# Optimization experiments

Measured on AMD Instinct MI355X. Metric: run time of the kernel, lower is better.

## Reference

```python
import jax, jax.numpy as jnp
import numpy as np
from jax import lax

B, S, D, H = 8, 1024, 512, 8
K = 25  # moving-average kernel
EPS = 1e-6


def setup_inputs() -> dict:
    key = jax.random.key(0)
    ks = jax.random.split(key, 8)

    def dense_w(k, din, dout):
        return (jax.random.normal(k, (din, dout), jnp.float32) / np.sqrt(din).astype(np.float32))

    return {
        "x": jax.random.normal(ks[0], (B, S, D), jnp.float32),
        "wq": dense_w(ks[1], D, D), "bq": jnp.zeros((D,), jnp.float32),
        "wk": dense_w(ks[2], D, D), "bk": jnp.zeros((D,), jnp.float32),
        "wv": dense_w(ks[3], D, D), "bv": jnp.zeros((D,), jnp.float32),
        "wo": dense_w(ks[4], D, D), "bo": jnp.zeros((D,), jnp.float32),
        "w1": dense_w(ks[5], D, 4 * D), "b1": jnp.zeros((4 * D,), jnp.float32),
        "w2": dense_w(ks[6], 4 * D, D), "b2": jnp.zeros((D,), jnp.float32),
        "g1": jnp.ones((D,), jnp.float32), "be1": jnp.zeros((D,), jnp.float32),
        "g2": jnp.ones((D,), jnp.float32), "be2": jnp.zeros((D,), jnp.float32),
        "g3": jnp.ones((D,), jnp.float32), "be3": jnp.zeros((D,), jnp.float32),
        "num_heads": H,
    }


def _moving_avg(x):
    # TF AveragePooling1D(pool=K, stride=1, padding='same'): divisor excludes padding.
    s = lax.reduce_window(x, 0.0, lax.add, (1, K, 1), (1, 1, 1), 'SAME')
    cnt = lax.reduce_window(jnp.ones((1, x.shape[1], 1), x.dtype), 0.0, lax.add,
                            (1, K, 1), (1, 1, 1), 'SAME')
    return s / cnt


def _layernorm(x, g, b):
    m = jnp.mean(x, -1, keepdims=True)
    v = jnp.var(x, -1, keepdims=True)
    return (x - m) * jax.lax.rsqrt(v + EPS) * g + b


def _auto_correlation(x, wq, bq, wk, bk, wv, bv, wo, bo, num_heads):
    b, s, d = x.shape
    dp = d // num_heads
    def split_heads(t):
        return t.reshape(b, s, num_heads, dp).transpose(0, 2, 1, 3)  # [B,H,S,dp]
    q = split_heads(x @ wq + bq)
    k = split_heads(x @ wk + bk)
    v = split_heads(x @ wv + bv)
    # Faithful to source: rfft over innermost (depth) axis, fft_length = 2*S.
    qf = jnp.fft.rfft(q, n=2 * s, axis=-1)
    kf = jnp.fft.rfft(k, n=2 * s, axis=-1)
    corr = jnp.fft.irfft(qf * jnp.conj(kf), n=2 * s, axis=-1)[..., :s]  # [B,H,S,S]
    scale = 1.0 / np.sqrt(dp).astype(np.float32)
    attn = jax.nn.softmax(scale * corr, axis=-1)
    out = jnp.einsum('bhst,bhtd->bhsd', attn, v)
    out = out.transpose(0, 2, 1, 3).reshape(b, s, d)
    return out @ wo + bo


def reference(x, wq, bq, wk, bk, wv, bv, wo, bo, w1, b1, w2, b2,
              g1, be1, g2, be2, g3, be3, num_heads):
    trend_init = _moving_avg(x)
    seasonal_init = x - trend_init
    attn_out = _auto_correlation(seasonal_init, wq, bq, wk, bk, wv, bv, wo, bo, num_heads)
    out1 = _layernorm(attn_out + seasonal_init, g1, be1)
    ffn = jax.nn.relu(out1 @ w1 + b1) @ w2 + b2
    seasonal_out = _layernorm(out1 + ffn, g2, be2) + seasonal_init
    trend2 = _moving_avg(seasonal_out)
    seasonal_final = seasonal_out - trend2
    x_out = seasonal_final + (trend2 + trend_init)
    return _layernorm(x_out, g3, be3)
```

## Files before the change

kernel.cpp:

```cpp
#include <hip/hip_runtime.h>
#include <cstdint>


typedef float f32x4 __attribute__((ext_vector_type(4)));
typedef __bf16 bf16x8 __attribute__((ext_vector_type(8)));
typedef _Float16 h2t __attribute__((ext_vector_type(2)));
typedef unsigned short u16;
typedef unsigned int u32;
typedef u32 u32x4 __attribute__((ext_vector_type(4)));

__device__ __forceinline__ u16 f2bf(float f) {
  unsigned int u = __float_as_uint(f);
  u = (u + 0x7FFFu + ((u >> 16) & 1u)) >> 16;
  return (u16)u;
}

__device__ __forceinline__ float bf2f(u16 b) { return __uint_as_float((u32)b << 16); }

__device__ __forceinline__ u16 f2h(float f) {
  _Float16 hv = (_Float16)f;
  u16 b;
  __builtin_memcpy(&b, &hv, 2);
  return b;
}

__device__ __forceinline__ float dot2h(u32 qp, u32 kp_, float c) {
#if __has_builtin(__builtin_amdgcn_fdot2)
  return __builtin_amdgcn_fdot2(__builtin_bit_cast(h2t, qp),
                                __builtin_bit_cast(h2t, kp_), c, false);
#else
  h2t q = __builtin_bit_cast(h2t, qp), k = __builtin_bit_cast(h2t, kp_);
  c = fmaf((float)q.x, (float)k.x, c);
  return fmaf((float)q.y, (float)k.y, c);
#endif
}

__device__ __forceinline__ void gload_lds16(const void* g, void* l) {
  __builtin_amdgcn_global_load_lds((__attribute__((address_space(1))) void*)g,
                                   (__attribute__((address_space(3))) void*)l,
                                   16, 0, 0);
}

__global__ __launch_bounds__(256) void prep_kernel(
    const float* __restrict__ wq, const float* __restrict__ wk,
    const float* __restrict__ wv, const float* __restrict__ wo,
    const float* __restrict__ w1, const float* __restrict__ w2,
    const float* __restrict__ bq, const float* __restrict__ bk,
    u16* __restrict__ wqkt, u16* __restrict__ wvt, u16* __restrict__ wot,
    u16* __restrict__ w1t, u16* __restrict__ w2t, float* __restrict__ qkbias,
    const float* __restrict__ x, u16* __restrict__ seas_bf,
    u16* __restrict__ a64, float* __restrict__ srow) {
  __shared__ float tile[32][33];
  int i = blockIdx.x;
  int tid = threadIdx.x;
  int tx = tid & 31, ty = tid >> 5;
  if (i >= 3076) {
    int blk = i - 3076;
    int sc = blk & 127, b = blk >> 7;
    int d = tid * 2;
    const float* xb = x + (size_t)b * 1024 * 512 + d;
    int s0 = sc * 8;
    int lo = max(s0 - 12, 0), hi = min(s0 + 12, 1023);
    float sx = 0.f, sy = 0.f;
    for (int j = lo; j <= hi; ++j) {
      float2 v = *(const float2*)&xb[(size_t)j * 512];
      sx += v.x;
      sy += v.y;
    }
    float ax = 0.f, ay = 0.f;
#pragma unroll
    for (int s = s0; s < s0 + 8; ++s) {
      int l2 = max(s - 12, 0), h2 = min(s + 12, 1023);
      float invc = 1.f / (float)(h2 - l2 + 1);
      float2 xv = *(const float2*)&xb[(size_t)s * 512];
      float sex = xv.x - sx * invc;
      float sey = xv.y - sy * invc;
      size_t idx = (size_t)(b * 1024 + s) * 512 + d;
      u32 pk = (u32)f2bf(sex) | ((u32)f2bf(sey) << 16);
      *(u32*)&seas_bf[idx] = pk;
      if (s < 64) *(u32*)&a64[(size_t)(b * 64 + s) * 512 + d] = pk;
      ax += sex;
      ay += sey;
      if (s - 12 >= 0) {
        float2 v = *(const float2*)&xb[(size_t)(s - 12) * 512];
        sx -= v.x;
        sy -= v.y;
      }
      if (s + 13 <= 1023) {
        float2 v = *(const float2*)&xb[(size_t)(s + 13) * 512];
        sx += v.x;
        sy += v.y;
      }
    }
    atomicAdd(&srow[b * 512 + d], ax);
    atomicAdd(&srow[b * 512 + d + 1], ay);
    return;
  }
  if (i >= 3072) {
    int idx = (i - 3072) * 256 + tid;
    qkbias[idx] = idx < 512 ? bq[idx] : bk[idx - 512];
    return;
  }
  const float* src;
  u16* dst;
  int R, C, bx, by;
  if (i < 1024) {
    int w = i >> 8, l = i & 255;
    src = (w == 0 ? wq : w == 1 ? wk : w == 2 ? wv : wo);
    dst = (w == 0 ? wqkt : w == 1 ? wqkt + 512 * 512 : w == 2 ? wvt : wot);
    R = 512; C = 512; bx = l & 15; by = l >> 4;
  } else if (i < 2048) {
    int l = i - 1024;
    src = w1; dst = w1t; R = 512; C = 2048; bx = l & 15; by = l >> 4;
  } else {
    int l = i - 2048;
    src = w2; dst = w2t; R = 2048; C = 512; bx = l & 63; by = l >> 6;
  }
  int r0 = bx * 32, c0 = by * 32;
#pragma unroll
  for (int k = 0; k < 4; ++k)
    tile[ty + 8 * k][tx] = src[(size_t)(r0 + ty + 8 * k) * C + c0 + tx];
  __syncthreads();
#pragma unroll
  for (int k = 0; k < 4; ++k)
    dst[(size_t)(c0 + ty + 8 * k) * R + r0 + tx] = f2bf(tile[tx][ty + 8 * k]);
}

__global__ __launch_bounds__(256) void vsum_kernel(
    const float* __restrict__ srow, const float* __restrict__ wv,
    const float* __restrict__ bv, float* __restrict__ vsum) {
  int blk = blockIdx.x;
  int b = blk >> 1;
  int n = (blk & 1) * 256 + threadIdx.x;
  float a0 = 0.f, a1 = 0.f, a2 = 0.f, a3 = 0.f;
  float a4 = 0.f, a5 = 0.f, a6 = 0.f, a7 = 0.f;
  const float* sr = srow + b * 512;
  for (int k = 0; k < 512; k += 8) {
    a0 = fmaf(sr[k + 0], wv[(size_t)(k + 0) * 512 + n], a0);
    a1 = fmaf(sr[k + 1], wv[(size_t)(k + 1) * 512 + n], a1);
    a2 = fmaf(sr[k + 2], wv[(size_t)(k + 2) * 512 + n], a2);
    a3 = fmaf(sr[k + 3], wv[(size_t)(k + 3) * 512 + n], a3);
    a4 = fmaf(sr[k + 4], wv[(size_t)(k + 4) * 512 + n], a4);
    a5 = fmaf(sr[k + 5], wv[(size_t)(k + 5) * 512 + n], a5);
    a6 = fmaf(sr[k + 6], wv[(size_t)(k + 6) * 512 + n], a6);
    a7 = fmaf(sr[k + 7], wv[(size_t)(k + 7) * 512 + n], a7);
  }
  vsum[b * 512 + n] = ((a0 + a1) + (a2 + a3)) + ((a4 + a5) + (a6 + a7)) + 1024.f * bv[n];
}

template <int RELU, int OMODE, int KSPLIT>
__global__ __launch_bounds__(512, 1) void gemm8p_kernel(
    const u16* __restrict__ A, const u16* __restrict__ Bt,
    const float* __restrict__ bias, void* __restrict__ Cv, void* __restrict__ Cv2,
    int M, int N, int K) {
  __shared__ u16 As[3][2][256 * 32];
  __shared__ u16 Bs[3][2][128 * 32];
  const int tid = threadIdx.x;
  const int wid = tid >> 6, lane = tid & 63;
  const int wm = wid >> 2, wn = wid & 3;
  const int la = lane & 15, lg = lane >> 4;
  int nwg = gridDim.x * gridDim.y;
  int lin = blockIdx.y * gridDim.x + blockIdx.x;
  int swz = (lin & 7) * (nwg >> 3) + (lin >> 3);
  int bx = swz / gridDim.y, by = swz % gridDim.y;
  const int row0 = bx * 256, col0 = by * 128;
  const int z = (KSPLIT > 1) ? (int)blockIdx.z : 0;
  const int kbeg = z * (K / KSPLIT);
  const int nt = (K / KSPLIT) / 64;
  f32x4 acc[8][2] = {};

  auto stageh = [&](int buf, int h, int k0) {
    int kh = k0 + h * 32;
    {
      int p = tid, r = p >> 2, cg = (p & 3) ^ ((r >> 1) & 3);
      gload_lds16(A + (size_t)(row0 + r) * K + kh + cg * 8,
                  ((char*)&As[buf][h][0]) + p * 16);
    }
    {
      int p = tid + 512, r = p >> 2, cg = (p & 3) ^ ((r >> 1) & 3);
      gload_lds16(A + (size_t)(row0 + r) * K + kh + cg * 8,
                  ((char*)&As[buf][h][0]) + p * 16);
    }
    {
      int p = tid, r = p >> 2, cg = (p & 3) ^ ((r >> 1) & 3);
      gload_lds16(Bt + (size_t)(col0 + r) * K + kh + cg * 8,
                  ((char*)&Bs[buf][h][0]) + p * 16);
    }
  };

  stageh(0, 0, kbeg);
  stageh(0, 1, kbeg);
  stageh(1, 0, kbeg + 64);
  stageh(1, 1, kbeg + 64);
  asm volatile("s_waitcnt vmcnt(6)" ::: "memory");
  __builtin_amdgcn_s_barrier();
  __builtin_amdgcn_sched_barrier(0);

  for (int t = 0; t < nt; ++t) {
    const int buf = t % 3;
    const int nbuf = (t + 2) % 3;
    const bool pre = (t + 2 < nt);
#pragma unroll
    for (int h = 0; h < 2; ++h) {
      bf16x8 af[8], bf[2];
#pragma unroll
      for (int mf = 0; mf < 8; ++mf) {
        int r = wm * 128 + mf * 16 + la;
        int cp = lg ^ ((r >> 1) & 3);
        af[mf] = *(const bf16x8*)&As[buf][h][r * 32 + cp * 8];
      }
#pragma unroll
      for (int nf = 0; nf < 2; ++nf) {
        int r = wn * 32 + nf * 16 + la;
        int cp = lg ^ ((r >> 1) & 3);
        bf[nf] = *(const bf16x8*)&Bs[buf][h][r * 32 + cp * 8];
      }
      if (pre) stageh(nbuf, h, kbeg + (t + 2) * 64);
      __builtin_amdgcn_sched_barrier(0);
      __builtin_amdgcn_s_barrier();
      __builtin_amdgcn_s_setprio(1);
#pragma unroll
      for (int mf = 0; mf < 8; ++mf)
#pragma unroll
        for (int nf = 0; nf < 2; ++nf)
          acc[mf][nf] = __builtin_amdgcn_mfma_f32_16x16x32_bf16(af[mf], bf[nf], acc[mf][nf], 0, 0, 0);
      __builtin_amdgcn_s_setprio(0);
      __builtin_amdgcn_sched_barrier(0);
      if (h == 0) __builtin_amdgcn_s_barrier();
    }
    if (pre)
      asm volatile("s_waitcnt vmcnt(6)" ::: "memory");
    else if (t + 1 < nt)
      asm volatile("s_waitcnt vmcnt(0)" ::: "memory");
    __builtin_amdgcn_s_barrier();
    __builtin_amdgcn_sched_barrier(0);
  }

  void* Cout = (z == 0) ? Cv : Cv2;
#pragma unroll
  for (int mf = 0; mf < 8; ++mf) {
    int r = row0 + wm * 128 + mf * 16 + lg * 4;
#pragma unroll
    for (int nf = 0; nf < 2; ++nf) {
      int cc = col0 + wn * 32 + nf * 16 + la;
      float bvv = (z == 0) ? bias[cc] : 0.f;
#pragma unroll
      for (int j = 0; j < 4; ++j) {
        float v = acc[mf][nf][j] + bvv;
        if (RELU) v = fmaxf(v, 0.f);
        if constexpr (OMODE == 1)
          ((u16*)Cout)[(size_t)(r + j) * N + cc] = f2bf(v);
        else
          ((u16*)Cout)[(size_t)(r + j) * N + cc] = f2h(v);
      }
    }
  }
}

template <int RELU>
__global__ __launch_bounds__(512, 1) void gemm256_kernel(
    const u16* __restrict__ A, const u16* __restrict__ Bt,
    const float* __restrict__ bias, u16* __restrict__ C, int M, int N, int K) {
  constexpr int BK = 32;
  __shared__ u16 As[3][256 * BK];
  __shared__ u16 Bs[3][256 * BK];
  const int tid = threadIdx.x;
  const int wid = tid >> 6, lane = tid & 63;
  const int wm = wid >> 2, wn = wid & 3;
  const int la = lane & 15, lg = lane >> 4;
  int nwg = gridDim.x * gridDim.y;
  int lin = blockIdx.y * gridDim.x + blockIdx.x;
  int swz = (lin & 7) * (nwg >> 3) + (lin >> 3);
  int bx = swz / gridDim.y, by = swz % gridDim.y;
  const int row0 = bx * 256, col0 = by * 256;
  const int nt = K / BK;
  f32x4 acc[8][4] = {};

  auto stage = [&](int buf, int k0) {
#pragma unroll
    for (int j = 0; j < 2; ++j) {
      int p = tid + j * 512;
      int r = p >> 2, cg = (p & 3) ^ ((r >> 1) & 3);
      gload_lds16(A + (size_t)(row0 + r) * K + k0 + cg * 8, ((char*)As[buf]) + p * 16);
      gload_lds16(Bt + (size_t)(col0 + r) * K + k0 + cg * 8, ((char*)Bs[buf]) + p * 16);
    }
  };

  stage(0, 0);
  stage(1, BK);
  asm volatile("s_waitcnt vmcnt(4)" ::: "memory");
  __builtin_amdgcn_s_barrier();
  __builtin_amdgcn_sched_barrier(0);

  for (int t = 0; t < nt; ++t) {
    const int cur = t % 3;
    if (t + 2 < nt) stage((t + 2) % 3, (t + 2) * BK);
    __builtin_amdgcn_sched_barrier(0);
    bf16x8 af[8], bfr[4];
#pragma unroll
    for (int mf = 0; mf < 8; ++mf) {
      int r = wm * 128 + mf * 16 + la;
      int cp = lg ^ ((r >> 1) & 3);
      af[mf] = *(const bf16x8*)(((const char*)As[cur]) + r * 64 + cp * 16);
    }
#pragma unroll
    for (int nf = 0; nf < 4; ++nf) {
      int r = wn * 64 + nf * 16 + la;
      int cp = lg ^ ((r >> 1) & 3);
      bfr[nf] = *(const bf16x8*)(((const char*)Bs[cur]) + r * 64 + cp * 16);
    }
    __builtin_amdgcn_s_setprio(1);
#pragma unroll
    for (int mf = 0; mf < 8; ++mf)
#pragma unroll
      for (int nf = 0; nf < 4; ++nf)
        acc[mf][nf] = __builtin_amdgcn_mfma_f32_16x16x32_bf16(af[mf], bfr[nf], acc[mf][nf], 0, 0, 0);
    __builtin_amdgcn_s_setprio(0);
    if (t + 2 < nt)
      asm volatile("s_waitcnt vmcnt(4)" ::: "memory");
    else
      asm volatile("s_waitcnt vmcnt(0)" ::: "memory");
    __builtin_amdgcn_s_barrier();
    __builtin_amdgcn_sched_barrier(0);
  }

#pragma unroll
  for (int mf = 0; mf < 8; ++mf) {
    int r = row0 + wm * 128 + mf * 16 + lg * 4;
#pragma unroll
    for (int nf = 0; nf < 4; ++nf) {
      int cc = col0 + wn * 64 + nf * 16 + la;
      float bvv = bias[cc];
#pragma unroll
      for (int j = 0; j < 4; ++j) {
        float v = acc[mf][nf][j] + bvv;
        if (RELU) v = fmaxf(v, 0.f);
        C[(size_t)(r + j) * N + cc] = f2bf(v);
      }
    }
  }
}

__global__ __launch_bounds__(256, 6) void gemm_v_kernel(
    const u16* __restrict__ A, const u16* __restrict__ Bt,
    const float* __restrict__ bias, u16* __restrict__ Cv, int M, int N, int K) {
  constexpr int BK = 32;
  __shared__ u16 As[2][128 * BK];
  __shared__ u16 Bs[2][64 * BK];
  const int tid = threadIdx.x;
  const int wid = tid >> 6, lane = tid & 63;
  const int wm = wid >> 1, wn = wid & 1;
  const int la = lane & 15, lg = lane >> 4;
  const int row0 = blockIdx.x * 128, col0 = blockIdx.y * 64;
  const int ksteps = K / BK;
  f32x4 acc[4][2] = {};

  auto stage = [&](int buf, int k0) {
    {
      int p = tid, r = p >> 2, cg = (p & 3) ^ ((r >> 1) & 3);
      gload_lds16(A + (size_t)(row0 + r) * K + k0 + cg * 8, ((char*)As[buf]) + p * 16);
    }
    {
      int p = tid + 256, r = p >> 2, cg = (p & 3) ^ ((r >> 1) & 3);
      gload_lds16(A + (size_t)(row0 + r) * K + k0 + cg * 8, ((char*)As[buf]) + p * 16);
    }
    {
      int p = tid, r = p >> 2, cg = (p & 3) ^ ((r >> 1) & 3);
      gload_lds16(Bt + (size_t)(col0 + r) * K + k0 + cg * 8, ((char*)Bs[buf]) + p * 16);
    }
  };

  stage(0, 0);
  __syncthreads();
  for (int t = 0; t < ksteps; ++t) {
    const int cur = t & 1;
    if (t + 1 < ksteps) stage(cur ^ 1, (t + 1) * BK);
    bf16x8 af[4], bfr[2];
#pragma unroll
    for (int m = 0; m < 4; ++m) {
      int r = wm * 64 + m * 16 + la;
      int cp = lg ^ ((r >> 1) & 3);
      af[m] = *(const bf16x8*)(((const char*)As[cur]) + r * 64 + cp * 16);
    }
#pragma unroll
    for (int n = 0; n < 2; ++n) {
      int r = wn * 32 + n * 16 + la;
      int cp = lg ^ ((r >> 1) & 3);
      bfr[n] = *(const bf16x8*)(((const char*)Bs[cur]) + r * 64 + cp * 16);
    }
#pragma unroll
    for (int m = 0; m < 4; ++m)
#pragma unroll
      for (int n = 0; n < 2; ++n)
        acc[m][n] = __builtin_amdgcn_mfma_f32_16x16x32_bf16(af[m], bfr[n], acc[m][n], 0, 0, 0);
    __syncthreads();
  }

#pragma unroll
  for (int m = 0; m < 4; ++m) {
    int r = row0 + wm * 64 + m * 16 + lg * 4;
#pragma unroll
    for (int n = 0; n < 2; ++n) {
      int cc = col0 + wn * 32 + n * 16 + la;
      float bvv = bias[cc];
#pragma unroll
      for (int j = 0; j < 4; ++j) {
        float v = acc[m][n][j] + bvv;
        int rr = r + j;
        int bb = rr >> 6, tt = rr & 63, hh = cc >> 6, dd = cc & 63;
        Cv[(((size_t)bb * 8 + hh) * 64 + dd) * 64 + tt] = f2bf(v);
      }
    }
  }
}

__global__ __launch_bounds__(256) void attn_mfma_kernel(
    const u16* __restrict__ qk, const u16* __restrict__ v64t,
    const float* __restrict__ vsum, u16* __restrict__ attn_bf) {
  __shared__ u32 qE[16][64];
  __shared__ u32 qO[16][64];
  __shared__ u32 kp[16][32];
  __shared__ u16 coef[16][64];
  __shared__ u16 vtt[64][64];
  __shared__ float zc[16];
  __shared__ float Vs[64];
  int bid = blockIdx.x;
  int scnk = bid & 63, h = (bid >> 6) & 7, b = bid >> 9;
  int tid = threadIdx.x, wid = tid >> 6, lane = tid & 63;
  int bh = b * 8 + h;
  int row0 = b * 1024 + scnk * 16;

  {
    int p = tid, r = p >> 3, cc = p & 7;
    gload_lds16(v64t + ((size_t)bh * 4096 + r * 64 + ((cc ^ (r & 7)) * 8)),
                ((char*)vtt) + p * 16);
    p = tid + 256; r = p >> 3; cc = p & 7;
    gload_lds16(v64t + ((size_t)bh * 4096 + r * 64 + ((cc ^ (r & 7)) * 8)),
                ((char*)vtt) + p * 16);
  }
  for (int idx = tid; idx < 512; idx += 256) {
    int s = idx >> 5, j = (idx & 31) + 32;
    qE[s][j] = 0;
  }
  {
    if (tid < 128) {
      int s = tid >> 3, c = tid & 7;
      size_t grow = ((size_t)(row0 + s)) * 1024 + h * 64;
      *(f32x4*)&qE[s][c * 4] = *(const f32x4*)&qk[grow + c * 8];
    } else {
      int t2 = tid - 128;
      int s = t2 >> 3, c = t2 & 7;
      size_t grow = ((size_t)(row0 + s)) * 1024 + 512 + h * 64;
      *(f32x4*)&kp[s][c * 4] = *(const f32x4*)&qk[grow + c * 8];
    }
  }
  if (tid < 64) Vs[tid] = vsum[b * 512 + h * 64 + tid];
  __syncthreads();
  for (int idx = tid; idx < 512; idx += 256) {
    int s = idx >> 5, j = idx & 31;
    u32 a = qE[s][j], b2 = qE[s][j + 1];
    qO[s][j] = (a >> 16) | (b2 << 16);
    qO[s][j + 32] = 0;
  }
  __syncthreads();
  for (int i = 0; i < 4; ++i) {
    int s = wid * 4 + i;
    u32x4 kk4[8];
#pragma unroll
    for (int u = 0; u < 8; ++u) kk4[u] = *(const u32x4*)&kp[s][u * 4];
    int t = lane, sel = t & 1;
    const u32* qptr = (sel ? qO[s] : qE[s]) + (t >> 1);
    float c = 0.f;
#pragma unroll
    for (int u = 0; u < 8; ++u) {
#pragma unroll
      for (int v = 0; v < 4; ++v) c = dot2h(qptr[u * 4 + v], kk4[u][v], c);
    }
    float sc = c * 0.125f;
    float mx = fmaxf(sc, 0.f);
#pragma unroll
    for (int off = 32; off >= 1; off >>= 1) mx = fmaxf(mx, __shfl_xor(mx, off));
    float w = __expf(sc - mx), wz = __expf(-mx);
    float sw = w;
#pragma unroll
    for (int off = 32; off >= 1; off >>= 1) sw += __shfl_xor(sw, off);
    float inv = 1.f / (sw + 960.f * wz);
    *(u16*)(((char*)&coef[s][0]) + ((2 * t) ^ ((s & 7) << 4))) = f2bf((w - wz) * inv);
    if (lane == 0) zc[s] = wz * inv;
  }
  __syncthreads();
  {
    int la = lane & 15, lg = lane >> 4;
    int r = la;
    int n0 = wid * 16 + la;
    f32x4 a0 = {};
#pragma unroll
    for (int ks = 0; ks < 2; ++ks) {
      int lr = ks * 4 + lg;
      bf16x8 af = *(const bf16x8*)(((const char*)coef) + r * 128 + ((lr ^ (r & 7)) << 4));
      bf16x8 b0 = *(const bf16x8*)(((const char*)vtt) + n0 * 128 + ((lr ^ (n0 & 7)) << 4));
      a0 = __builtin_amdgcn_mfma_f32_16x16x32_bf16(af, b0, a0, 0, 0, 0);
    }
    int srl0 = lg * 4;
    float vs0 = Vs[wid * 16 + la];
#pragma unroll
    for (int j = 0; j < 4; ++j) {
      size_t rb = (size_t)(row0 + srl0 + j) * 512 + h * 64;
      attn_bf[rb + wid * 16 + la] = f2bf(a0[j] + zc[srl0 + j] * vs0);
    }
  }
}

__device__ __forceinline__ void block_reduce_2(float& a, float& b, float* sbuf) {
  int tid = threadIdx.x, wid = tid >> 6, lane = tid & 63;
#pragma unroll
  for (int off = 32; off >= 1; off >>= 1) {
    a += __shfl_xor(a, off);
    b += __shfl_xor(b, off);
  }
  if (lane == 0) {
    sbuf[wid] = a;
    sbuf[4 + wid] = b;
  }
  __syncthreads();
  a = sbuf[0] + sbuf[1] + sbuf[2] + sbuf[3];
  b = sbuf[4] + sbuf[5] + sbuf[6] + sbuf[7];
  __syncthreads();
}

__global__ __launch_bounds__(256) void ln_res_kernel(
    const u16* __restrict__ xa, const u16* __restrict__ xb,
    u16* __restrict__ res_out,
    const float* __restrict__ g, const float* __restrict__ be) {
  __shared__ float sbuf[8];
  int row = blockIdx.x, tid = threadIdx.x;
  int d = tid * 2;
  size_t base = (size_t)row * 512 + d;
  u32 pa = *(const u32*)&xa[base];
  u32 pb = *(const u32*)&xb[base];
  u32 pr = *(const u32*)&res_out[base];
  float v0 = bf2f((u16)pa) + bf2f((u16)pb) + bf2f((u16)pr);
  float v1 = bf2f((u16)(pa >> 16)) + bf2f((u16)(pb >> 16)) + bf2f((u16)(pr >> 16));
  float s = v0 + v1, q = v0 * v0 + v1 * v1;
  block_reduce_2(s, q, sbuf);
  float mean = s * (1.f / 512.f);
  float var = q * (1.f / 512.f) - mean * mean;
  float rs = rsqrtf(var + 1e-6f);
  float2 gg = *(const float2*)&g[d];
  float2 bb = *(const float2*)&be[d];
  float o0 = (v0 - mean) * rs * gg.x + bb.x;
  float o1 = (v1 - mean) * rs * gg.y + bb.y;
  *(u32*)&res_out[base] = (u32)f2bf(o0) | ((u32)f2bf(o1) << 16);
}

__global__ __launch_bounds__(256) void final_kernel(
    const u16* __restrict__ out1, const u16* __restrict__ fa,
    const u16* __restrict__ fb, const float* __restrict__ x,
    const float* __restrict__ g2, const float* __restrict__ be2,
    const float* __restrict__ g3, const float* __restrict__ be3,
    float* __restrict__ out) {
  __shared__ float sbuf[8];
  int row = blockIdx.x, tid = threadIdx.x;
  int d = tid * 2;
  size_t base = (size_t)row * 512 + d;
  u32 po = *(const u32*)&out1[base];
  u32 pa = *(const u32*)&fa[base];
  u32 pb = *(const u32*)&fb[base];
  float t0 = bf2f((u16)po) + bf2f((u16)pa) + bf2f((u16)pb);
  float t1 = bf2f((u16)(po >> 16)) + bf2f((u16)(pa >> 16)) + bf2f((u16)(pb >> 16));
  float s = t0 + t1, q = t0 * t0 + t1 * t1;
  block_reduce_2(s, q, sbuf);
  float mean = s * (1.f / 512.f);
  float var = q * (1.f / 512.f) - mean * mean;
  float rs = rsqrtf(var + 1e-6f);
  float2 g2v = *(const float2*)&g2[d];
  float2 b2v = *(const float2*)&be2[d];
  float2 xv = *(const float2*)&x[base];
  float y0 = (t0 - mean) * rs * g2v.x + b2v.x + xv.x;
  float y1 = (t1 - mean) * rs * g2v.y + b2v.y + xv.y;
  s = y0 + y1;
  q = y0 * y0 + y1 * y1;
  block_reduce_2(s, q, sbuf);
  mean = s * (1.f / 512.f);
  var = q * (1.f / 512.f) - mean * mean;
  rs = rsqrtf(var + 1e-6f);
  float2 g3v = *(const float2*)&g3[d];
  float2 b3v = *(const float2*)&be3[d];
  float2 o = make_float2((y0 - mean) * rs * g3v.x + b3v.x,
                         (y1 - mean) * rs * g3v.y + b3v.y);
  *(float2*)&out[base] = o;
}

extern "C" void kernel_launch(void* const* d_in, const int* in_sizes, int n_in,
                              void* d_out, int out_size, void* d_ws, size_t ws_size,
                              hipStream_t stream) {
  const float* x = (const float*)d_in[0];
  const float* wq = (const float*)d_in[1];
  const float* bq = (const float*)d_in[2];
  const float* wk = (const float*)d_in[3];
  const float* bk = (const float*)d_in[4];
  const float* wv = (const float*)d_in[5];
  const float* bv = (const float*)d_in[6];
  const float* wo = (const float*)d_in[7];
  const float* bo = (const float*)d_in[8];
  const float* w1 = (const float*)d_in[9];
  const float* b1 = (const float*)d_in[10];
  const float* w2 = (const float*)d_in[11];
  const float* b2 = (const float*)d_in[12];
  const float* g1 = (const float*)d_in[13];
  const float* be1 = (const float*)d_in[14];
  const float* g2 = (const float*)d_in[15];
  const float* be2 = (const float*)d_in[16];
  const float* g3 = (const float*)d_in[17];
  const float* be3 = (const float*)d_in[18];
  float* out = (float*)d_out;

  const size_t MS = 8192ull * 512ull;
  float* srow = (float*)d_ws;
  float* vsumb = srow + 4096;
  float* qkbias = vsumb + 4096;
  u16* qk_f16 = (u16*)(qkbias + 1024);
  u16* hidden = qk_f16 + 8192ull * 1024;
  u16* seas_bf = hidden + 8192ull * 2048;
  u16* attn_bf = seas_bf + MS;
  u16* wo0 = attn_bf + MS;
  u16* wo1 = wo0 + MS;
  u16* v64t = wo1 + MS;
  u16* a64_bf = v64t + 512 * 512;
  u16* wqkt = a64_bf + 512 * 512;
  u16* wvt = wqkt + 1024 * 512;
  u16* wot = wvt + 512 * 512;
  u16* w1t = wot + 512 * 512;
  u16* w2t = w1t + 2048ull * 512;
  u16* ff0 = qk_f16;
  u16* ff1 = ff0 + MS;

  hipMemsetAsync(srow, 0, 4096 * sizeof(float), stream);
  prep_kernel<<<4100, 256, 0, stream>>>(
      wq, wk, wv, wo, w1, w2, bq, bk, wqkt, wvt, wot, w1t, w2t, qkbias,
      x, seas_bf, a64_bf, srow);
  vsum_kernel<<<16, 256, 0, stream>>>(srow, wv, bv, vsumb);

  gemm8p_kernel<0, 2, 1><<<dim3(32, 8), 512, 0, stream>>>(
      seas_bf, wqkt, qkbias, qk_f16, nullptr, 8192, 1024, 512);
  gemm_v_kernel<<<dim3(4, 8), 256, 0, stream>>>(a64_bf, wvt, bv, v64t, 512, 512, 512);

  attn_mfma_kernel<<<4096, 256, 0, stream>>>(qk_f16, v64t, vsumb, attn_bf);

  gemm8p_kernel<0, 1, 2><<<dim3(32, 4, 2), 512, 0, stream>>>(
      attn_bf, wot, bo, wo0, wo1, 8192, 512, 512);
  ln_res_kernel<<<8192, 256, 0, stream>>>(wo0, wo1, seas_bf, g1, be1);

  gemm256_kernel<1><<<dim3(32, 8), 512, 0, stream>>>(
      seas_bf, w1t, b1, hidden, 8192, 2048, 512);
  gemm8p_kernel<0, 1, 2><<<dim3(32, 4, 2), 512, 0, stream>>>(
      hidden, w2t, b2, ff0, ff1, 8192, 512, 2048);

  final_kernel<<<8192, 256, 0, stream>>>(seas_bf, ff0, ff1, x, g2, be2, g3, be3, out);
}
```

Baseline: 203.5 us.

## Rewrite FFN GEMMs with ping-pong 64-wide K pipeline and 4-way split-K for W2

Replaces the triple-buffered 256x256 GEMM with a double-buffered kernel that stages 64-wide K chunks as two 32-wide sub-slabs. Global loads for the next chunk are interleaved between half-tile MFMA phases, with barriers and priority hints around each phase, so that loads overlap compute. The same kernel now also runs the second FFN GEMM as a 4-way split-K over 256x256 tiles, replacing the 2-way gemm8p launch. The extra partial outputs reuse the wo0/wo1 buffers and are summed in final_kernel. The aim is better load/compute overlap and more workgroups for the K=2048 GEMM, at the cost of extra bf16 partial-sum traffic and barriers.

```diff
diff --git a/kernel.cpp b/kernel.cpp
--- a/kernel.cpp
+++ b/kernel.cpp
@@ -257,13 +257,13 @@
   }
 }
 
-template <int RELU>
-__global__ __launch_bounds__(512, 1) void gemm256_kernel(
+template <int RELU, int KSPLIT>
+__global__ __launch_bounds__(512, 1) void gemmfp_kernel(
     const u16* __restrict__ A, const u16* __restrict__ Bt,
-    const float* __restrict__ bias, u16* __restrict__ C, int M, int N, int K) {
-  constexpr int BK = 32;
-  __shared__ u16 As[3][256 * BK];
-  __shared__ u16 Bs[3][256 * BK];
+    const float* __restrict__ bias, u16* __restrict__ C0, u16* __restrict__ C1,
+    u16* __restrict__ C2, u16* __restrict__ C3, int M, int N, int K) {
+  __shared__ u16 As[2][2][256 * 32];
+  __shared__ u16 Bs[2][2][256 * 32];
   const int tid = threadIdx.x;
   const int wid = tid >> 6, lane = tid & 63;
   const int wm = wid >> 2, wn = wid & 3;
@@ -273,69 +273,111 @@
   int swz = (lin & 7) * (nwg >> 3) + (lin >> 3);
   int bx = swz / gridDim.y, by = swz % gridDim.y;
   const int row0 = bx * 256, col0 = by * 256;
-  const int nt = K / BK;
+  const int z = (KSPLIT > 1) ? (int)blockIdx.z : 0;
+  const int kbeg = z * (K / KSPLIT);
+  const int nt = (K / KSPLIT) / 64;
   f32x4 acc[8][4] = {};
 
-  auto stage = [&](int buf, int k0) {
+  auto stageA = [&](int d, int s, int k0) {
 #pragma unroll
     for (int j = 0; j < 2; ++j) {
       int p = tid + j * 512;
       int r = p >> 2, cg = (p & 3) ^ ((r >> 1) & 3);
-      gload_lds16(A + (size_t)(row0 + r) * K + k0 + cg * 8, ((char*)As[buf]) + p * 16);
-      gload_lds16(Bt + (size_t)(col0 + r) * K + k0 + cg * 8, ((char*)Bs[buf]) + p * 16);
+      gload_lds16(A + (size_t)(row0 + r) * K + k0 + s * 32 + cg * 8,
+                  ((char*)&As[d][s][0]) + p * 16);
     }
   };
-
-  stage(0, 0);
-  stage(1, BK);
-  asm volatile("s_waitcnt vmcnt(4)" ::: "memory");
+  auto stageB = [&](int d, int s, int k0) {
+#pragma unroll
+    for (int j = 0; j < 2; ++j) {
+      int p = tid + j * 512;
+      int r = p >> 2, cg = (p & 3) ^ ((r >> 1) & 3);
+      gload_lds16(Bt + (size_t)(col0 + r) * K + k0 + s * 32 + cg * 8,
+                  ((char*)&Bs[d][s][0]) + p * 16);
+    }
+  };
+
+  stageA(0, 0, kbeg);
+  stageB(0, 0, kbeg);
+  stageA(0, 1, kbeg);
+  stageB(0, 1, kbeg);
+  asm volatile("s_waitcnt vmcnt(0)" ::: "memory");
   __builtin_amdgcn_s_barrier();
   __builtin_amdgcn_sched_barrier(0);
 
   for (int t = 0; t < nt; ++t) {
-    const int cur = t % 3;
-    if (t + 2 < nt) stage((t + 2) % 3, (t + 2) * BK);
-    __builtin_amdgcn_sched_barrier(0);
-    bf16x8 af[8], bfr[4];
-#pragma unroll
-    for (int mf = 0; mf < 8; ++mf) {
-      int r = wm * 128 + mf * 16 + la;
-      int cp = lg ^ ((r >> 1) & 3);
-      af[mf] = *(const bf16x8*)(((const char*)As[cur]) + r * 64 + cp * 16);
-    }
-#pragma unroll
-    for (int nf = 0; nf < 4; ++nf) {
-      int r = wn * 64 + nf * 16 + la;
-      int cp = lg ^ ((r >> 1) & 3);
-      bfr[nf] = *(const bf16x8*)(((const char*)Bs[cur]) + r * 64 + cp * 16);
-    }
-    __builtin_amdgcn_s_setprio(1);
-#pragma unroll
-    for (int mf = 0; mf < 8; ++mf)
-#pragma unroll
-      for (int nf = 0; nf < 4; ++nf)
-        acc[mf][nf] = __builtin_amdgcn_mfma_f32_16x16x32_bf16(af[mf], bfr[nf], acc[mf][nf], 0, 0, 0);
-    __builtin_amdgcn_s_setprio(0);
-    if (t + 2 < nt)
-      asm volatile("s_waitcnt vmcnt(4)" ::: "memory");
-    else
-      asm volatile("s_waitcnt vmcnt(0)" ::: "memory");
-    __builtin_amdgcn_s_barrier();
-    __builtin_amdgcn_sched_barrier(0);
-  }
-
+    const int d = t & 1, nd = d ^ 1;
+    const int k1 = kbeg + (t + 1) * 64;
+    const bool pre = (t + 1 < nt);
+    bf16x8 af[8], bf[2];
+#pragma unroll
+    for (int s = 0; s < 2; ++s) {
+#pragma unroll
+      for (int mf = 0; mf < 8; ++mf) {
+        int r = wm * 128 + mf * 16 + la;
+        int cp = lg ^ ((r >> 1) & 3);
+        af[mf] = *(const bf16x8*)(((const char*)&As[d][s][0]) + r * 64 + cp * 16);
+      }
+#pragma unroll
+      for (int nf = 0; nf < 2; ++nf) {
+        int r = wn * 64 + nf * 16 + la;
+        int cp = lg ^ ((r >> 1) & 3);
+        bf[nf] = *(const bf16x8*)(((const char*)&Bs[d][s][0]) + r * 64 + cp * 16);
+      }
+      if (pre) stageA(nd, s, k1);
+      __builtin_amdgcn_sched_barrier(0);
+      __builtin_amdgcn_s_barrier();
+      asm volatile("s_waitcnt lgkmcnt(0)" ::: "memory");
+      __builtin_amdgcn_sched_barrier(0);
+      __builtin_amdgcn_s_setprio(1);
+#pragma unroll
+      for (int mf = 0; mf < 8; ++mf)
+#pragma unroll
+        for (int nf = 0; nf < 2; ++nf)
+          acc[mf][nf] = __builtin_amdgcn_mfma_f32_16x16x32_bf16(af[mf], bf[nf], acc[mf][nf], 0, 0, 0);
+      __builtin_amdgcn_s_setprio(0);
+      __builtin_amdgcn_sched_barrier(0);
+      __builtin_amdgcn_s_barrier();
+#pragma unroll
+      for (int nf = 0; nf < 2; ++nf) {
+        int r = wn * 64 + (nf + 2) * 16 + la;
+        int cp = lg ^ ((r >> 1) & 3);
+        bf[nf] = *(const bf16x8*)(((const char*)&Bs[d][s][0]) + r * 64 + cp * 16);
+      }
+      if (pre) stageB(nd, s, k1);
+      __builtin_amdgcn_sched_barrier(0);
+      if (pre)
+        asm volatile("s_waitcnt vmcnt(4)" ::: "memory");
+      else
+        asm volatile("s_waitcnt vmcnt(0)" ::: "memory");
+      __builtin_amdgcn_s_barrier();
+      asm volatile("s_waitcnt lgkmcnt(0)" ::: "memory");
+      __builtin_amdgcn_sched_barrier(0);
+      __builtin_amdgcn_s_setprio(1);
+#pragma unroll
+      for (int mf = 0; mf < 8; ++mf)
+#pragma unroll
+        for (int nf = 0; nf < 2; ++nf)
+          acc[mf][nf + 2] = __builtin_amdgcn_mfma_f32_16x16x32_bf16(af[mf], bf[nf], acc[mf][nf + 2], 0, 0, 0);
+      __builtin_amdgcn_s_setprio(0);
+      __builtin_amdgcn_sched_barrier(0);
+      __builtin_amdgcn_s_barrier();
+    }
+  }
+
+  u16* Cout = (z == 0) ? C0 : (z == 1) ? C1 : (z == 2) ? C2 : C3;
 #pragma unroll
   for (int mf = 0; mf < 8; ++mf) {
     int r = row0 + wm * 128 + mf * 16 + lg * 4;
 #pragma unroll
     for (int nf = 0; nf < 4; ++nf) {
       int cc = col0 + wn * 64 + nf * 16 + la;
-      float bvv = bias[cc];
+      float bvv = (z == 0) ? bias[cc] : 0.f;
 #pragma unroll
       for (int j = 0; j < 4; ++j) {
         float v = acc[mf][nf][j] + bvv;
         if (RELU) v = fmaxf(v, 0.f);
-        C[(size_t)(r + j) * N + cc] = f2bf(v);
+        Cout[(size_t)(r + j) * N + cc] = f2bf(v);
       }
     }
   }
@@ -555,7 +597,8 @@
 
 __global__ __launch_bounds__(256) void final_kernel(
     const u16* __restrict__ out1, const u16* __restrict__ fa,
-    const u16* __restrict__ fb, const float* __restrict__ x,
+    const u16* __restrict__ fb, const u16* __restrict__ fc,
+    const u16* __restrict__ fd, const float* __restrict__ x,
     const float* __restrict__ g2, const float* __restrict__ be2,
     const float* __restrict__ g3, const float* __restrict__ be3,
     float* __restrict__ out) {
@@ -566,8 +609,11 @@
   u32 po = *(const u32*)&out1[base];
   u32 pa = *(const u32*)&fa[base];
   u32 pb = *(const u32*)&fb[base];
-  float t0 = bf2f((u16)po) + bf2f((u16)pa) + bf2f((u16)pb);
-  float t1 = bf2f((u16)(po >> 16)) + bf2f((u16)(pa >> 16)) + bf2f((u16)(pb >> 16));
+  u32 pc = *(const u32*)&fc[base];
+  u32 pd = *(const u32*)&fd[base];
+  float t0 = bf2f((u16)po) + bf2f((u16)pa) + bf2f((u16)pb) + bf2f((u16)pc) + bf2f((u16)pd);
+  float t1 = bf2f((u16)(po >> 16)) + bf2f((u16)(pa >> 16)) + bf2f((u16)(pb >> 16)) +
+             bf2f((u16)(pc >> 16)) + bf2f((u16)(pd >> 16));
   float s = t0 + t1, q = t0 * t0 + t1 * t1;
   block_reduce_2(s, q, sbuf);
   float mean = s * (1.f / 512.f);
@@ -634,6 +680,8 @@
   u16* w2t = w1t + 2048ull * 512;
   u16* ff0 = qk_f16;
   u16* ff1 = ff0 + MS;
+  u16* ff2 = wo0;
+  u16* ff3 = wo1;
 
   hipMemsetAsync(srow, 0, 4096 * sizeof(float), stream);
   prep_kernel<<<4100, 256, 0, stream>>>(
@@ -651,10 +699,11 @@
       attn_bf, wot, bo, wo0, wo1, 8192, 512, 512);
   ln_res_kernel<<<8192, 256, 0, stream>>>(wo0, wo1, seas_bf, g1, be1);
 
-  gemm256_kernel<1><<<dim3(32, 8), 512, 0, stream>>>(
-      seas_bf, w1t, b1, hidden, 8192, 2048, 512);
-  gemm8p_kernel<0, 1, 2><<<dim3(32, 4, 2), 512, 0, stream>>>(
-      hidden, w2t, b2, ff0, ff1, 8192, 512, 2048);
-
-  final_kernel<<<8192, 256, 0, stream>>>(seas_bf, ff0, ff1, x, g2, be2, g3, be3, out);
-}
+  gemmfp_kernel<1, 1><<<dim3(32, 8), 512, 0, stream>>>(
+      seas_bf, w1t, b1, hidden, nullptr, nullptr, nullptr, 8192, 2048, 512);
+  gemmfp_kernel<0, 4><<<dim3(32, 2, 4), 512, 0, stream>>>(
+      hidden, w2t, b2, ff0, ff1, ff2, ff3, 8192, 512, 2048);
+
+  final_kernel<<<8192, 256, 0, stream>>>(seas_bf, ff0, ff1, ff2, ff3, x,
+                                         g2, be2, g3, be3, out);
+}
```

Result: faster. 199.1 us (-2.2%).
